# Kernel tuning notes

Hardware: AMD Instinct MI355X
Metric: run time of the kernel (lower is better)

The kernel has to match this reference:

```python
import jax, jax.numpy as jnp
import numpy as np

B, LIN, E, D, N = 32, 2048, 512, 512, 2  # batch, enc len, enc hidden, dec hidden, dec layers


def setup_inputs() -> dict:
    key = jax.random.key(0)
    k1, k2, k3, k4, k5 = jax.random.split(key, 5)
    d_hidden = jax.random.normal(k1, (B, N, D), dtype=jnp.float32)
    encoder_outputs = jax.random.normal(k2, (B, LIN, E), dtype=jnp.float32)
    fan_in = E + N * D
    lim1 = 1.0 / np.sqrt(fan_in)
    W1 = jax.random.uniform(k3, (fan_in, D), minval=-lim1, maxval=lim1, dtype=jnp.float32)
    b1 = jax.random.uniform(k4, (D,), minval=-lim1, maxval=lim1, dtype=jnp.float32)
    lim2 = 1.0 / np.sqrt(D)
    w2 = jax.random.uniform(k5, (D,), minval=-lim2, maxval=lim2, dtype=jnp.float32)
    return {"d_hidden": d_hidden, "encoder_outputs": encoder_outputs,
            "W1": W1, "b1": b1, "w2": w2}


def reference(d_hidden, encoder_outputs, W1, b1, w2):
    # Faithful to: tanh(Linear(cat(repeat(d_hidden), enc))) -> Linear(.,1) -> softmax
    # cat@W1 == d_flat@W1_d + enc@W1_e (broadcast-add avoids materializing the concat).
    nd = d_hidden.shape[1] * d_hidden.shape[2]
    d_flat = d_hidden.reshape(d_hidden.shape[0], nd)        # [B, N*D]
    W1_d, W1_e = W1[:nd], W1[nd:]                            # [N*D,D], [E,D]
    dec_proj = d_flat @ W1_d + b1                            # [B, D]
    enc_proj = jnp.einsum('ble,ed->bld', encoder_outputs, W1_e)  # [B, Lin, D]
    attn_hidden = jnp.tanh(enc_proj + dec_proj[:, None, :])  # [B, Lin, D]
    scores = jnp.einsum('bld,d->bl', attn_hidden, w2)        # [B, Lin]
    return jax.nn.softmax(scores, axis=-1)
```

## Files before the change

### kernel.cpp

```cpp
#include <hip/hip_runtime.h>
#include <hip/hip_bf16.h>

#define L_SZ 2048
#define E_SZ 512
#define D_SZ 512
#define ND   1024
#define WS_DEC_OFF 0
#define WS_BT_OFF  (32*512*4)
#define WS_SC_OFF  (32*512*4 + 512*512*2)

typedef unsigned short ushort_t;
typedef unsigned int   uint_t;
typedef __attribute__((ext_vector_type(8))) short short8;
typedef __attribute__((ext_vector_type(4))) float floatx4;

__device__ __forceinline__ ushort_t f2bf(float f) {
  uint_t u = __builtin_bit_cast(uint_t, f);
  u += 0x7fffu + ((u >> 16) & 1u);
  return (ushort_t)(u >> 16);
}

__device__ __forceinline__ float fast_tanh(float x) {
  float e = __expf(2.0f * x);
  return 1.0f - 2.0f * __builtin_amdgcn_rcpf(e + 1.0f);
}

__device__ __forceinline__ void dma16(const ushort_t* g, ushort_t* l) {
  __builtin_amdgcn_global_load_lds(
      (const __attribute__((address_space(1))) uint_t*)(const void*)g,
      (__attribute__((address_space(3))) uint_t*)(void*)l,
      16, 0, 0);
}

__global__ __launch_bounds__(256) void prep_k(const float* __restrict__ dh,
                                              const float* __restrict__ W1,
                                              const float* __restrict__ b1,
                                              float* __restrict__ dec,
                                              ushort_t* __restrict__ Bt) {
  int blk = blockIdx.x, t = threadIdx.x;
  if (blk < 256) {
    int b = blk >> 3, d = (blk & 7) * 64 + (t & 63);
    int q = t >> 6;
    __shared__ float red[4][64];
    const float* dfb = dh + b * ND;
    float s = 0.f;
    #pragma unroll 8
    for (int k = q * 256; k < q * 256 + 256; k++)
      s = fmaf(dfb[k], W1[k * D_SZ + d], s);
    red[q][t & 63] = s;
    __syncthreads();
    if (q == 0)
      dec[b * D_SZ + d] = red[0][t] + red[1][t] + red[2][t] + red[3][t] + b1[d];
  } else {
    int tid = blk - 256;
    int tk = (tid >> 4) * 32, tn = (tid & 15) * 32;
    __shared__ float tile[32][33];
    int cc = t & 31, r8 = t >> 5;
    #pragma unroll
    for (int p = 0; p < 4; p++) {
      int r = r8 + p * 8;
      tile[r][cc] = W1[(ND + tk + r) * D_SZ + tn + cc];
    }
    __syncthreads();
    #pragma unroll
    for (int p = 0; p < 4; p++) {
      int nn = r8 + p * 8;
      Bt[(tn + nn) * E_SZ + tk + cc] = f2bf(tile[cc][nn]);
    }
  }
}

__global__ __launch_bounds__(512, 2) void main_k(const float* __restrict__ enc,
                                                 const ushort_t* __restrict__ Bt,
                                                 const float* __restrict__ dec,
                                                 const float* __restrict__ w2,
                                                 float* __restrict__ scores) {
  const int b  = blockIdx.y;
  const int l0 = blockIdx.x * 64;
  const int t  = threadIdx.x;
  const int wave = t >> 6, lane = t & 63;
  const int col = lane & 15, quad = lane >> 4;

  __shared__ __align__(16) ushort_t Bs[2][512 * 64];
  __shared__ __align__(16) ushort_t As[2][64 * 64];
  __shared__ float s_sc[64];

  if (t < 64) s_sc[t] = 0.f;

  floatx4 acc[4][4];
  #pragma unroll
  for (int mt = 0; mt < 4; mt++)
    #pragma unroll
    for (int nt = 0; nt < 4; nt++)
      acc[mt][nt] = (floatx4){0.f, 0.f, 0.f, 0.f};

  const float* arow = enc + (size_t)(b * L_SZ + l0) * E_SZ;

  const int am = t >> 3, ac = t & 7;
  const float* aptr = arow + am * E_SZ + ac * 8;
  const int awoff = am * 64 + ((ac ^ (am & 7)) << 3);

  const int bn0 = wave * 64 + (lane >> 3);
  const int bc0 = (lane & 7) ^ ((lane >> 3) & 7);
  const ushort_t* bptr0 = Bt + bn0 * E_SZ + bc0 * 8;

  float4 pa = *(const float4*)aptr;
  float4 pb = *(const float4*)(aptr + 4);
  #pragma unroll
  for (int j = 0; j < 8; j++)
    dma16(bptr0 + j * 8 * E_SZ, &Bs[0][wave * 4096 + j * 512]);
  {
    union { short8 v; __hip_bfloat162 h[4]; } pk;
    pk.h[0] = __float22bfloat162_rn(make_float2(pa.x, pa.y));
    pk.h[1] = __float22bfloat162_rn(make_float2(pa.z, pa.w));
    pk.h[2] = __float22bfloat162_rn(make_float2(pb.x, pb.y));
    pk.h[3] = __float22bfloat162_rn(make_float2(pb.z, pb.w));
    *(short8*)&As[0][awoff] = pk.v;
  }
  asm volatile("s_waitcnt vmcnt(0) lgkmcnt(0)" ::: "memory");
  __builtin_amdgcn_s_barrier();
  __builtin_amdgcn_sched_barrier(0);

  #pragma unroll 1
  for (int kw = 0; kw < 8; kw++) {
    const ushort_t* Acur = &As[kw & 1][0];
    const ushort_t* Bcur = &Bs[kw & 1][0];

    if (kw < 7) {
      const float* ap = aptr + (kw + 1) * 64;
      pa = *(const float4*)ap;
      pb = *(const float4*)(ap + 4);
      const ushort_t* bp = bptr0 + (kw + 1) * 64;
      ushort_t* bld = &Bs[(kw + 1) & 1][wave * 4096];
      #pragma unroll
      for (int j = 0; j < 8; j++)
        dma16(bp + j * 8 * E_SZ, bld + j * 512);
    }

    #pragma unroll
    for (int ks = 0; ks < 2; ks++) {
      short8 af[4], bfr[4];
      #pragma unroll
      for (int mt = 0; mt < 4; mt++) {
        int m = mt * 16 + col;
        af[mt] = *(const short8*)&Acur[m * 64 + ((((ks << 2) + quad) ^ (m & 7)) << 3)];
      }
      #pragma unroll
      for (int nt = 0; nt < 4; nt++) {
        int n = wave * 64 + nt * 16 + col;
        bfr[nt] = *(const short8*)&Bcur[n * 64 + ((((ks << 2) + quad) ^ (n & 7)) << 3)];
      }
      #pragma unroll
      for (int mt = 0; mt < 4; mt++)
        #pragma unroll
        for (int nt = 0; nt < 4; nt++)
          acc[mt][nt] = __builtin_amdgcn_mfma_f32_16x16x32_bf16(af[mt], bfr[nt], acc[mt][nt], 0, 0, 0);
    }

    if (kw < 7) {
      union { short8 v; __hip_bfloat162 h[4]; } pk;
      pk.h[0] = __float22bfloat162_rn(make_float2(pa.x, pa.y));
      pk.h[1] = __float22bfloat162_rn(make_float2(pa.z, pa.w));
      pk.h[2] = __float22bfloat162_rn(make_float2(pb.x, pb.y));
      pk.h[3] = __float22bfloat162_rn(make_float2(pb.z, pb.w));
      *(short8*)&As[(kw + 1) & 1][awoff] = pk.v;
    }

    asm volatile("s_waitcnt vmcnt(0) lgkmcnt(0)" ::: "memory");
    __builtin_amdgcn_s_barrier();
    __builtin_amdgcn_sched_barrier(0);
  }

  const float* decb = dec + b * D_SZ;
  float sums[4][4];
  #pragma unroll
  for (int mt = 0; mt < 4; mt++)
    #pragma unroll
    for (int r = 0; r < 4; r++) sums[mt][r] = 0.f;

  #pragma unroll
  for (int nt = 0; nt < 4; nt++) {
    int n = wave * 64 + nt * 16 + col;
    float dv = decb[n];
    float wv = w2[n];
    #pragma unroll
    for (int mt = 0; mt < 4; mt++)
      #pragma unroll
      for (int r = 0; r < 4; r++)
        sums[mt][r] += fast_tanh(acc[mt][nt][r] + dv) * wv;
  }
  #pragma unroll
  for (int mt = 0; mt < 4; mt++) {
    #pragma unroll
    for (int r = 0; r < 4; r++) {
      float v = sums[mt][r];
      v += __shfl_xor(v, 1, 16);
      v += __shfl_xor(v, 2, 16);
      v += __shfl_xor(v, 4, 16);
      v += __shfl_xor(v, 8, 16);
      if (col == 0) atomicAdd(&s_sc[mt * 16 + quad * 4 + r], v);
    }
  }
  __syncthreads();
  if (t < 64) scores[b * L_SZ + l0 + t] = s_sc[t];
}

__global__ __launch_bounds__(1024) void softmax_k(const float* __restrict__ sc,
                                                  float* __restrict__ out) {
  int b = blockIdx.x, t = threadIdx.x;
  int wave = t >> 6, lane = t & 63;
  __shared__ float redm[16], reds[16];
  const float* row = sc + b * L_SZ;
  float v0 = row[t], v1 = row[t + 1024];
  float mx = fmaxf(v0, v1);
  #pragma unroll
  for (int off = 32; off >= 1; off >>= 1) mx = fmaxf(mx, __shfl_xor(mx, off, 64));
  if (lane == 0) redm[wave] = mx;
  __syncthreads();
  float m = redm[0];
  #pragma unroll
  for (int i = 1; i < 16; i++) m = fmaxf(m, redm[i]);
  v0 = __expf(v0 - m);
  v1 = __expf(v1 - m);
  float s = v0 + v1;
  #pragma unroll
  for (int off = 32; off >= 1; off >>= 1) s += __shfl_xor(s, off, 64);
  if (lane == 0) reds[wave] = s;
  __syncthreads();
  float sum = reds[0];
  #pragma unroll
  for (int i = 1; i < 16; i++) sum += reds[i];
  float inv = 1.0f / sum;
  out[b * L_SZ + t]        = v0 * inv;
  out[b * L_SZ + t + 1024] = v1 * inv;
}

extern "C" void kernel_launch(void* const* d_in, const int* in_sizes, int n_in,
                              void* d_out, int out_size, void* d_ws, size_t ws_size,
                              hipStream_t stream) {
  const float* d_hidden = (const float*)d_in[0];
  const float* enc      = (const float*)d_in[1];
  const float* W1       = (const float*)d_in[2];
  const float* b1       = (const float*)d_in[3];
  const float* w2       = (const float*)d_in[4];
  float* out = (float*)d_out;

  char* ws = (char*)d_ws;
  float*    dec = (float*)(ws + WS_DEC_OFF);
  ushort_t* Bt  = (ushort_t*)(ws + WS_BT_OFF);
  float*    sc  = (float*)(ws + WS_SC_OFF);

  prep_k<<<512, 256, 0, stream>>>(d_hidden, W1, b1, dec, Bt);
  main_k<<<dim3(32, 32), 512, 0, stream>>>(enc, Bt, dec, w2, sc);
  softmax_k<<<32, 1024, 0, stream>>>(sc, out);
}
```

Before: 263.9 us.

## Enlarge main GEMM tile to 128 rows with 16 waves and K-step 32

The main kernel now processes 128 encoder rows per block with 1024 threads (16 waves in a 2x8 grid), halving the number of blocks. Each block loads the bf16 W1_e tile once for twice as many rows, which halves total B-matrix traffic. The K step shrinks from 64 to 32, so there are 16 iterations with one MFMA k-slice each. The XOR swizzle on LDS is dropped, and that may add bank conflicts. The extra barriers per unit of work and the 512-block grid on 256 CUs may hurt latency hiding.

```diff
diff --git a/kernel.cpp b/kernel.cpp
--- a/kernel.cpp
+++ b/kernel.cpp
@@ -12,6 +12,7 @@
 typedef unsigned short ushort_t;
 typedef unsigned int   uint_t;
 typedef __attribute__((ext_vector_type(8))) short short8;
+typedef __attribute__((ext_vector_type(4))) short short4_t;
 typedef __attribute__((ext_vector_type(4))) float floatx4;
 
 __device__ __forceinline__ ushort_t f2bf(float f) {
@@ -70,22 +71,24 @@
   }
 }
 
-__global__ __launch_bounds__(512, 2) void main_k(const float* __restrict__ enc,
-                                                 const ushort_t* __restrict__ Bt,
-                                                 const float* __restrict__ dec,
-                                                 const float* __restrict__ w2,
-                                                 float* __restrict__ scores) {
+__global__ __launch_bounds__(1024, 4) void main_k(const float* __restrict__ enc,
+                                                  const ushort_t* __restrict__ Bt,
+                                                  const float* __restrict__ dec,
+                                                  const float* __restrict__ w2,
+                                                  float* __restrict__ scores) {
   const int b  = blockIdx.y;
-  const int l0 = blockIdx.x * 64;
+  const int l0 = blockIdx.x * 128;
   const int t  = threadIdx.x;
   const int wave = t >> 6, lane = t & 63;
   const int col = lane & 15, quad = lane >> 4;
-
-  __shared__ __align__(16) ushort_t Bs[2][512 * 64];
-  __shared__ __align__(16) ushort_t As[2][64 * 64];
-  __shared__ float s_sc[64];
-
-  if (t < 64) s_sc[t] = 0.f;
+  const int mbase = (wave >> 3) * 64;
+  const int nbase = (wave & 7) * 64;
+
+  __shared__ __align__(16) ushort_t Bs[2][512 * 32];
+  __shared__ __align__(16) ushort_t As[2][128 * 32];
+  __shared__ float s_sc[128];
+
+  if (t < 128) s_sc[t] = 0.f;
 
   floatx4 acc[4][4];
   #pragma unroll
@@ -96,74 +99,58 @@
 
   const float* arow = enc + (size_t)(b * L_SZ + l0) * E_SZ;
 
-  const int am = t >> 3, ac = t & 7;
-  const float* aptr = arow + am * E_SZ + ac * 8;
-  const int awoff = am * 64 + ((ac ^ (am & 7)) << 3);
-
-  const int bn0 = wave * 64 + (lane >> 3);
-  const int bc0 = (lane & 7) ^ ((lane >> 3) & 7);
-  const ushort_t* bptr0 = Bt + bn0 * E_SZ + bc0 * 8;
+  const int ar = t >> 3, akc = t & 7;
+  const float* aptr = arow + ar * E_SZ + akc * 4;
+  const int awoff = ar * 32 + akc * 4;
+
+  const int s0 = wave * 128 + lane;
+  const ushort_t* bsrc0 = Bt + (s0 >> 2) * E_SZ + (s0 & 3) * 8;
+  const int s1 = s0 + 64;
+  const ushort_t* bsrc1 = Bt + (s1 >> 2) * E_SZ + (s1 & 3) * 8;
 
   float4 pa = *(const float4*)aptr;
-  float4 pb = *(const float4*)(aptr + 4);
-  #pragma unroll
-  for (int j = 0; j < 8; j++)
-    dma16(bptr0 + j * 8 * E_SZ, &Bs[0][wave * 4096 + j * 512]);
+  dma16(bsrc0, &Bs[0][wave * 1024]);
+  dma16(bsrc1, &Bs[0][wave * 1024 + 512]);
   {
-    union { short8 v; __hip_bfloat162 h[4]; } pk;
+    union { short4_t v; __hip_bfloat162 h[2]; } pk;
     pk.h[0] = __float22bfloat162_rn(make_float2(pa.x, pa.y));
     pk.h[1] = __float22bfloat162_rn(make_float2(pa.z, pa.w));
-    pk.h[2] = __float22bfloat162_rn(make_float2(pb.x, pb.y));
-    pk.h[3] = __float22bfloat162_rn(make_float2(pb.z, pb.w));
-    *(short8*)&As[0][awoff] = pk.v;
+    *(short4_t*)&As[0][awoff] = pk.v;
   }
   asm volatile("s_waitcnt vmcnt(0) lgkmcnt(0)" ::: "memory");
   __builtin_amdgcn_s_barrier();
   __builtin_amdgcn_sched_barrier(0);
 
   #pragma unroll 1
-  for (int kw = 0; kw < 8; kw++) {
+  for (int kw = 0; kw < 16; kw++) {
     const ushort_t* Acur = &As[kw & 1][0];
     const ushort_t* Bcur = &Bs[kw & 1][0];
 
-    if (kw < 7) {
-      const float* ap = aptr + (kw + 1) * 64;
-      pa = *(const float4*)ap;
-      pb = *(const float4*)(ap + 4);
-      const ushort_t* bp = bptr0 + (kw + 1) * 64;
-      ushort_t* bld = &Bs[(kw + 1) & 1][wave * 4096];
+    if (kw < 15) {
+      pa = *(const float4*)(aptr + (kw + 1) * 32);
+      ushort_t* bld = &Bs[(kw + 1) & 1][wave * 1024];
+      dma16(bsrc0 + (kw + 1) * 32, bld);
+      dma16(bsrc1 + (kw + 1) * 32, bld + 512);
+    }
+
+    short8 af[4], bfr[4];
+    #pragma unroll
+    for (int mt = 0; mt < 4; mt++)
+      af[mt] = *(const short8*)&Acur[(mbase + mt * 16 + col) * 32 + quad * 8];
+    #pragma unroll
+    for (int nt = 0; nt < 4; nt++)
+      bfr[nt] = *(const short8*)&Bcur[(nbase + nt * 16 + col) * 32 + quad * 8];
+    #pragma unroll
+    for (int mt = 0; mt < 4; mt++)
       #pragma unroll
-      for (int j = 0; j < 8; j++)
-        dma16(bp + j * 8 * E_SZ, bld + j * 512);
-    }
-
-    #pragma unroll
-    for (int ks = 0; ks < 2; ks++) {
-      short8 af[4], bfr[4];
-      #pragma unroll
-      for (int mt = 0; mt < 4; mt++) {
-        int m = mt * 16 + col;
-        af[mt] = *(const short8*)&Acur[m * 64 + ((((ks << 2) + quad) ^ (m & 7)) << 3)];
-      }
-      #pragma unroll
-      for (int nt = 0; nt < 4; nt++) {
-        int n = wave * 64 + nt * 16 + col;
-        bfr[nt] = *(const short8*)&Bcur[n * 64 + ((((ks << 2) + quad) ^ (n & 7)) << 3)];
-      }
-      #pragma unroll
-      for (int mt = 0; mt < 4; mt++)
-        #pragma unroll
-        for (int nt = 0; nt < 4; nt++)
-          acc[mt][nt] = __builtin_amdgcn_mfma_f32_16x16x32_bf16(af[mt], bfr[nt], acc[mt][nt], 0, 0, 0);
-    }
-
-    if (kw < 7) {
-      union { short8 v; __hip_bfloat162 h[4]; } pk;
+      for (int nt = 0; nt < 4; nt++)
+        acc[mt][nt] = __builtin_amdgcn_mfma_f32_16x16x32_bf16(af[mt], bfr[nt], acc[mt][nt], 0, 0, 0);
+
+    if (kw < 15) {
+      union { short4_t v; __hip_bfloat162 h[2]; } pk;
       pk.h[0] = __float22bfloat162_rn(make_float2(pa.x, pa.y));
       pk.h[1] = __float22bfloat162_rn(make_float2(pa.z, pa.w));
-      pk.h[2] = __float22bfloat162_rn(make_float2(pb.x, pb.y));
-      pk.h[3] = __float22bfloat162_rn(make_float2(pb.z, pb.w));
-      *(short8*)&As[(kw + 1) & 1][awoff] = pk.v;
+      *(short4_t*)&As[(kw + 1) & 1][awoff] = pk.v;
     }
 
     asm volatile("s_waitcnt vmcnt(0) lgkmcnt(0)" ::: "memory");
@@ -180,7 +167,7 @@
 
   #pragma unroll
   for (int nt = 0; nt < 4; nt++) {
-    int n = wave * 64 + nt * 16 + col;
+    int n = nbase + nt * 16 + col;
     float dv = decb[n];
     float wv = w2[n];
     #pragma unroll
@@ -198,11 +185,11 @@
       v += __shfl_xor(v, 2, 16);
       v += __shfl_xor(v, 4, 16);
       v += __shfl_xor(v, 8, 16);
-      if (col == 0) atomicAdd(&s_sc[mt * 16 + quad * 4 + r], v);
+      if (col == 0) atomicAdd(&s_sc[mbase + mt * 16 + quad * 4 + r], v);
     }
   }
   __syncthreads();
-  if (t < 64) scores[b * L_SZ + l0 + t] = s_sc[t];
+  if (t < 128) scores[b * L_SZ + l0 + t] = s_sc[t];
 }
 
 __global__ __launch_bounds__(1024) void softmax_k(const float* __restrict__ sc,
@@ -251,6 +238,6 @@
   float*    sc  = (float*)(ws + WS_SC_OFF);
 
   prep_k<<<512, 256, 0, stream>>>(d_hidden, W1, b1, dec, Bt);
-  main_k<<<dim3(32, 32), 512, 0, stream>>>(enc, Bt, dec, w2, sc);
+  main_k<<<dim3(16, 32), 1024, 0, stream>>>(enc, Bt, dec, w2, sc);
   softmax_k<<<32, 1024, 0, stream>>>(sc, out);
 }
```

New measurement: 255.7 us. 1.03x faster.
